# Kernel tuning notes

Hardware: AMD Instinct MI355X
Metric: run time of the kernel (lower is better)

The kernel has to match this reference:

```python
import jax, jax.numpy as jnp
import numpy as np

DIM = 2048
NUM_HEADS = 16
HEAD_DIM = DIM // NUM_HEADS  # 128


def setup_inputs() -> dict:
    key = jax.random.key(0)
    ks = jax.random.split(key, 5)
    scale = 0.02
    x = jax.random.normal(ks[0], (1, 2048, DIM), dtype=jnp.float32)
    # nn.Linear weights stored as [out_features, in_features]
    Wq = jax.random.normal(ks[1], (DIM, DIM), dtype=jnp.float32) * scale
    Wk = jax.random.normal(ks[2], (HEAD_DIM, DIM), dtype=jnp.float32) * scale
    Wv = jax.random.normal(ks[3], (HEAD_DIM, DIM), dtype=jnp.float32) * scale
    Wo = jax.random.normal(ks[4], (DIM, DIM), dtype=jnp.float32) * scale
    return {"x": x, "Wq": Wq, "Wk": Wk, "Wv": Wv, "Wo": Wo}


def reference(x, Wq, Wk, Wv, Wo):
    batch, seq_len, dim = x.shape
    q = x @ Wq.T                                   # [b, s, dim]
    k = x @ Wk.T                                   # [b, s, head_dim] (shared across heads)
    v = x @ Wv.T                                   # [b, s, head_dim]
    q = q.reshape(batch, seq_len, NUM_HEADS, HEAD_DIM).transpose(0, 2, 1, 3)  # [b, h, s, d]
    # MQA: single KV head broadcast across query heads (no materialized repeat)
    scores = jnp.einsum("bhqd,bkd->bhqk", q, k) / (HEAD_DIM ** 0.5)
    probs = jax.nn.softmax(scores, axis=-1)        # [b, h, q, k]
    out = jnp.einsum("bhqk,bkd->bhqd", probs, v)   # [b, h, s, d]
    out = out.transpose(0, 2, 1, 3).reshape(batch, seq_len, dim)
    return out @ Wo.T
```

## Files before the change

### kernel.cpp

```cpp
#include <hip/hip_runtime.h>

typedef float  float4_t __attribute__((ext_vector_type(4)));
typedef __bf16 bf16x8   __attribute__((ext_vector_type(8)));
typedef unsigned short u16;

__device__ __forceinline__ u16 f2bf(float f) {
    unsigned u = __float_as_uint(f);
    u += 0x7fffu + ((u >> 16) & 1u);
    return (u16)(u >> 16);
}

#define GLOAD_LDS16(g, l)                                              \
    __builtin_amdgcn_global_load_lds(                                  \
        (__attribute__((address_space(1))) void*)(g),                  \
        (__attribute__((address_space(3))) void*)(l), 16, 0, 0)

__global__ __launch_bounds__(256) void cast_kernel(const float* __restrict__ in,
                                                   u16* __restrict__ out, int n4) {
    int i = blockIdx.x * 256 + threadIdx.x;
    if (i >= n4) return;
    float4 f = ((const float4*)in)[i];
    ushort4 r;
    r.x = f2bf(f.x); r.y = f2bf(f.y); r.z = f2bf(f.z); r.w = f2bf(f.w);
    ((ushort4*)out)[i] = r;
}

template <typename EPI>
__device__ __forceinline__ void gemm_core(const u16* __restrict__ A,
                                          const u16* __restrict__ B,
                                          int K, int bm, int bn, EPI epi) {
    __shared__ __align__(16) u16 As[128 * 32];
    __shared__ __align__(16) u16 Bs[128 * 32];
    const int tid  = threadIdx.x;
    const int lane = tid & 63, wave = tid >> 6;
    const int wm = wave >> 1, wn = wave & 1;
    const int quad = lane >> 4, l16 = lane & 15;

    float4_t acc[4][4] = {};
    const int r0 = tid >> 2;
    const int c0 = (tid & 3) * 8;

    for (int k0 = 0; k0 < K; k0 += 32) {
#pragma unroll
        for (int i = 0; i < 2; ++i) {
            const int row = i * 64 + r0;
            const int e   = (i * 256 + tid) * 8;
            GLOAD_LDS16(A + (size_t)(bm + row) * K + k0 + c0, &As[e]);
            GLOAD_LDS16(B + (size_t)(bn + row) * K + k0 + c0, &Bs[e]);
        }
        __syncthreads();

        bf16x8 af[4], bfr[4];
#pragma unroll
        for (int mi = 0; mi < 4; ++mi)
            af[mi] = *(const bf16x8*)&As[(wm * 64 + mi * 16 + l16) * 32 + quad * 8];
#pragma unroll
        for (int ni = 0; ni < 4; ++ni)
            bfr[ni] = *(const bf16x8*)&Bs[(wn * 64 + ni * 16 + l16) * 32 + quad * 8];
#pragma unroll
        for (int mi = 0; mi < 4; ++mi)
#pragma unroll
            for (int ni = 0; ni < 4; ++ni)
                acc[mi][ni] = __builtin_amdgcn_mfma_f32_16x16x32_bf16(
                    af[mi], bfr[ni], acc[mi][ni], 0, 0, 0);
        __syncthreads();
    }

#pragma unroll
    for (int mi = 0; mi < 4; ++mi) {
        const int row = bm + wm * 64 + mi * 16 + quad * 4;
#pragma unroll
        for (int ni = 0; ni < 4; ++ni) {
            const int col = bn + wn * 64 + ni * 16 + l16;
#pragma unroll
            for (int r = 0; r < 4; ++r) epi(row + r, col, acc[mi][ni][r]);
        }
    }
}

__global__ __launch_bounds__(256) void gemm_qkv(const u16* __restrict__ A,
                                                const u16* __restrict__ B,
                                                u16* __restrict__ qb,
                                                u16* __restrict__ kb,
                                                u16* __restrict__ vtb) {
    gemm_core(A, B, 2048, blockIdx.x * 128, blockIdx.y * 128,
              [=](int row, int col, float v) {
                  if (col < 2048)
                      qb[(size_t)row * 2048 + col] = f2bf(v * 0.08838834764831845f);
                  else if (col < 2176)
                      kb[(size_t)row * 128 + (col - 2048)] = f2bf(v);
                  else
                      vtb[(size_t)(col - 2176) * 2048 + row] = f2bf(v);
              });
}

__global__ __launch_bounds__(256) void gemm_out(const u16* __restrict__ A,
                                                const u16* __restrict__ B,
                                                float* __restrict__ C) {
    gemm_core(A, B, 2048, blockIdx.x * 128, blockIdx.y * 128,
              [=](int row, int col, float v) {
                  C[(size_t)row * 2048 + col] = v;
              });
}

__global__ __launch_bounds__(256) void mqa_attn(const u16* __restrict__ Q,
                                                const u16* __restrict__ Kmat,
                                                const u16* __restrict__ Vt,
                                                u16* __restrict__ O) {
    __shared__ __align__(16) u16 Ks[2][4][64 * 32];
    __shared__ __align__(16) u16 Vts[2][2][128 * 32];
    __shared__ __align__(16) u16 Ps[4][32 * 72];
    const int tid  = threadIdx.x;
    const int wave = tid >> 6, lane = tid & 63;
    const int quad = lane >> 4, l16 = lane & 15;
    const int h     = blockIdx.y;
    const int qbase = blockIdx.x * 128 + wave * 32;

    const int kr = tid >> 2, kc = (tid & 3) * 8;

    bf16x8 qf[2][4];
#pragma unroll
    for (int mt = 0; mt < 2; ++mt)
#pragma unroll
        for (int kb4 = 0; kb4 < 4; ++kb4)
            qf[mt][kb4] = *(const bf16x8*)(Q + (size_t)(qbase + mt * 16 + l16) * 2048 +
                                           h * 128 + kb4 * 32 + quad * 8);

    float4_t acc[2][8];
#pragma unroll
    for (int mt = 0; mt < 2; ++mt)
#pragma unroll
        for (int nt = 0; nt < 8; ++nt) acc[mt][nt] = (float4_t){0.f, 0.f, 0.f, 0.f};
    float lsum[8] = {};

    u16* pb = Ps[wave];

#pragma unroll
    for (int kb4 = 0; kb4 < 4; ++kb4)
        GLOAD_LDS16(Kmat + (size_t)kr * 128 + kb4 * 32 + kc, &Ks[0][kb4][tid * 8]);
#pragma unroll
    for (int kk = 0; kk < 2; ++kk)
#pragma unroll
        for (int h2 = 0; h2 < 2; ++h2)
            GLOAD_LDS16(Vt + (size_t)(h2 * 64 + kr) * 2048 + kk * 32 + kc,
                        &Vts[0][kk][(h2 * 64 + kr) * 32 + kc]);
    __syncthreads();

    int buf = 0;
    for (int s = 0; s < 32; ++s) {
        const int k0 = s * 64;
        if (s < 31) {
            const int kn = k0 + 64;
#pragma unroll
            for (int kb4 = 0; kb4 < 4; ++kb4)
                GLOAD_LDS16(Kmat + (size_t)(kn + kr) * 128 + kb4 * 32 + kc,
                            &Ks[buf ^ 1][kb4][tid * 8]);
#pragma unroll
            for (int kk = 0; kk < 2; ++kk)
#pragma unroll
                for (int h2 = 0; h2 < 2; ++h2)
                    GLOAD_LDS16(Vt + (size_t)(h2 * 64 + kr) * 2048 + kn + kk * 32 + kc,
                                &Vts[buf ^ 1][kk][(h2 * 64 + kr) * 32 + kc]);
        }

#pragma unroll
        for (int ct = 0; ct < 4; ++ct) {
            float4_t s0 = (float4_t){0.f, 0.f, 0.f, 0.f};
            float4_t s1 = (float4_t){0.f, 0.f, 0.f, 0.f};
#pragma unroll
            for (int kb4 = 0; kb4 < 4; ++kb4) {
                bf16x8 kf = *(const bf16x8*)&Ks[buf][kb4][(ct * 16 + l16) * 32 + quad * 8];
                s0 = __builtin_amdgcn_mfma_f32_16x16x32_bf16(qf[0][kb4], kf, s0, 0, 0, 0);
                s1 = __builtin_amdgcn_mfma_f32_16x16x32_bf16(qf[1][kb4], kf, s1, 0, 0, 0);
            }
#pragma unroll
            for (int r = 0; r < 4; ++r) {
                const float e0 = __expf(s0[r]);
                const float e1 = __expf(s1[r]);
                lsum[r]     += e0;
                lsum[4 + r] += e1;
                pb[(quad * 4 + r) * 72 + ct * 16 + l16]        = f2bf(e0);
                pb[(16 + quad * 4 + r) * 72 + ct * 16 + l16]   = f2bf(e1);
            }
        }
        bf16x8 pa[2][2];
#pragma unroll
        for (int mt = 0; mt < 2; ++mt)
#pragma unroll
            for (int kk = 0; kk < 2; ++kk)
                pa[mt][kk] = *(const bf16x8*)&pb[(mt * 16 + l16) * 72 + kk * 32 + quad * 8];
#pragma unroll
        for (int kk = 0; kk < 2; ++kk)
#pragma unroll
            for (int nt = 0; nt < 8; ++nt) {
                bf16x8 vf = *(const bf16x8*)&Vts[buf][kk][(nt * 16 + l16) * 32 + quad * 8];
                acc[0][nt] = __builtin_amdgcn_mfma_f32_16x16x32_bf16(pa[0][kk], vf, acc[0][nt], 0, 0, 0);
                acc[1][nt] = __builtin_amdgcn_mfma_f32_16x16x32_bf16(pa[1][kk], vf, acc[1][nt], 0, 0, 0);
            }
        __syncthreads();
        buf ^= 1;
    }

#pragma unroll
    for (int mt = 0; mt < 2; ++mt)
#pragma unroll
        for (int r = 0; r < 4; ++r) {
            float lrow = lsum[mt * 4 + r];
#pragma unroll
            for (int off = 1; off < 16; off <<= 1) lrow += __shfl_xor(lrow, off);
            const float inv = 1.0f / lrow;
            const size_t rowoff = (size_t)(qbase + mt * 16 + quad * 4 + r) * 2048 + h * 128;
#pragma unroll
            for (int nt = 0; nt < 8; ++nt)
                O[rowoff + nt * 16 + l16] = f2bf(acc[mt][nt][r] * inv);
        }
}

extern "C" void kernel_launch(void* const* d_in, const int* in_sizes, int n_in,
                              void* d_out, int out_size, void* d_ws, size_t ws_size,
                              hipStream_t stream) {
    const float* x  = (const float*)d_in[0];
    const float* Wq = (const float*)d_in[1];
    const float* Wk = (const float*)d_in[2];
    const float* Wv = (const float*)d_in[3];
    const float* Wo = (const float*)d_in[4];
    float* out = (float*)d_out;

    u16* ws   = (u16*)d_ws;
    u16* xb   = ws;
    u16* Wqb  = xb  + (4 << 20);
    u16* Wkb  = Wqb + (4 << 20);
    u16* Wvb  = Wkb + (256 << 10);
    u16* Wob  = Wvb + (256 << 10);
    u16* qb   = Wob + (4 << 20);
    u16* kb   = qb  + (4 << 20);
    u16* vtb  = kb  + (256 << 10);
    u16* attn = vtb + (256 << 10);

    cast_kernel<<<4096, 256, 0, stream>>>(x,  xb,  1 << 20);
    cast_kernel<<<4096, 256, 0, stream>>>(Wq, Wqb, 1 << 20);
    cast_kernel<<<256,  256, 0, stream>>>(Wk, Wkb, 1 << 16);
    cast_kernel<<<256,  256, 0, stream>>>(Wv, Wvb, 1 << 16);
    cast_kernel<<<4096, 256, 0, stream>>>(Wo, Wob, 1 << 20);

    gemm_qkv<<<dim3(16, 18), 256, 0, stream>>>(xb, Wqb, qb, kb, vtb);
    mqa_attn<<<dim3(16, 16), 256, 0, stream>>>(qb, kb, vtb, attn);
    gemm_out<<<dim3(16, 16), 256, 0, stream>>>(attn, Wob, out);
}
```

Measured before the change: 264.5 us.

## Fuse cast launches and shrink attention blocks to 128 threads without double buffering

Merges the five fp32-to-bf16 cast launches into a single kernel that picks its source tensor from the block index, removing per-launch overhead. The attention kernel now runs 64 query rows per 128-thread block, doubling the grid to 512 blocks for better CU coverage on the 256-CU part. It drops K/V double buffering in favour of single-buffered loads followed by a barrier. This lowers LDS use per block but exposes global load latency unless other resident blocks hide it, and each K/V tile is now loaded twice as often across the grid.

```diff
diff --git a/kernel.cpp b/kernel.cpp
--- a/kernel.cpp
+++ b/kernel.cpp
@@ -15,14 +15,27 @@
         (__attribute__((address_space(1))) void*)(g),                  \
         (__attribute__((address_space(3))) void*)(l), 16, 0, 0)
 
-__global__ __launch_bounds__(256) void cast_kernel(const float* __restrict__ in,
-                                                   u16* __restrict__ out, int n4) {
-    int i = blockIdx.x * 256 + threadIdx.x;
-    if (i >= n4) return;
-    float4 f = ((const float4*)in)[i];
+__global__ __launch_bounds__(256) void cast_all(const float* __restrict__ x,
+                                                const float* __restrict__ wq,
+                                                const float* __restrict__ wk,
+                                                const float* __restrict__ wv,
+                                                const float* __restrict__ wo,
+                                                u16* __restrict__ xb, u16* __restrict__ wqb,
+                                                u16* __restrict__ wkb, u16* __restrict__ wvb,
+                                                u16* __restrict__ wob) {
+    const int b = blockIdx.x;
+    const float* src;
+    u16* dst;
+    int i;
+    if (b < 4096)      { src = x;  dst = xb;  i = b * 256 + threadIdx.x; }
+    else if (b < 8192) { src = wq; dst = wqb; i = (b - 4096) * 256 + threadIdx.x; }
+    else if (b < 8448) { src = wk; dst = wkb; i = (b - 8192) * 256 + threadIdx.x; }
+    else if (b < 8704) { src = wv; dst = wvb; i = (b - 8448) * 256 + threadIdx.x; }
+    else               { src = wo; dst = wob; i = (b - 8704) * 256 + threadIdx.x; }
+    float4 f = ((const float4*)src)[i];
     ushort4 r;
     r.x = f2bf(f.x); r.y = f2bf(f.y); r.z = f2bf(f.z); r.w = f2bf(f.w);
-    ((ushort4*)out)[i] = r;
+    ((ushort4*)dst)[i] = r;
 }
 
 template <typename EPI>
@@ -103,20 +116,18 @@
               });
 }
 
-__global__ __launch_bounds__(256) void mqa_attn(const u16* __restrict__ Q,
-                                                const u16* __restrict__ Kmat,
-                                                const u16* __restrict__ Vt,
-                                                u16* __restrict__ O) {
-    __shared__ __align__(16) u16 Ks[2][4][64 * 32];
-    __shared__ __align__(16) u16 Vts[2][2][128 * 32];
-    __shared__ __align__(16) u16 Ps[4][32 * 72];
+__global__ __launch_bounds__(128, 2) void mqa_attn(const u16* __restrict__ Q,
+                                                   const u16* __restrict__ Kmat,
+                                                   const u16* __restrict__ Vt,
+                                                   u16* __restrict__ O) {
+    __shared__ __align__(16) u16 Ks[4 * 64 * 32];
+    __shared__ __align__(16) u16 Vts[2 * 128 * 32];
+    __shared__ __align__(16) u16 Ps[2][32 * 72];
     const int tid  = threadIdx.x;
     const int wave = tid >> 6, lane = tid & 63;
     const int quad = lane >> 4, l16 = lane & 15;
     const int h     = blockIdx.y;
-    const int qbase = blockIdx.x * 128 + wave * 32;
-
-    const int kr = tid >> 2, kc = (tid & 3) * 8;
+    const int qbase = blockIdx.x * 64 + wave * 32;
 
     bf16x8 qf[2][4];
 #pragma unroll
@@ -135,33 +146,23 @@
 
     u16* pb = Ps[wave];
 
-#pragma unroll
-    for (int kb4 = 0; kb4 < 4; ++kb4)
-        GLOAD_LDS16(Kmat + (size_t)kr * 128 + kb4 * 32 + kc, &Ks[0][kb4][tid * 8]);
-#pragma unroll
-    for (int kk = 0; kk < 2; ++kk)
-#pragma unroll
-        for (int h2 = 0; h2 < 2; ++h2)
-            GLOAD_LDS16(Vt + (size_t)(h2 * 64 + kr) * 2048 + kk * 32 + kc,
-                        &Vts[0][kk][(h2 * 64 + kr) * 32 + kc]);
-    __syncthreads();
-
-    int buf = 0;
     for (int s = 0; s < 32; ++s) {
         const int k0 = s * 64;
-        if (s < 31) {
-            const int kn = k0 + 64;
-#pragma unroll
-            for (int kb4 = 0; kb4 < 4; ++kb4)
-                GLOAD_LDS16(Kmat + (size_t)(kn + kr) * 128 + kb4 * 32 + kc,
-                            &Ks[buf ^ 1][kb4][tid * 8]);
-#pragma unroll
-            for (int kk = 0; kk < 2; ++kk)
-#pragma unroll
-                for (int h2 = 0; h2 < 2; ++h2)
-                    GLOAD_LDS16(Vt + (size_t)(h2 * 64 + kr) * 2048 + kn + kk * 32 + kc,
-                                &Vts[buf ^ 1][kk][(h2 * 64 + kr) * 32 + kc]);
-        }
+#pragma unroll
+        for (int i = 0; i < 8; ++i) {
+            const int slot = i * 128 + tid;
+            const int sub = slot >> 8, win = slot & 255;
+            const int row = win >> 2, ch = (win & 3) * 8;
+            GLOAD_LDS16(Kmat + (size_t)(k0 + row) * 128 + sub * 32 + ch, &Ks[slot * 8]);
+        }
+#pragma unroll
+        for (int i = 0; i < 8; ++i) {
+            const int slot = i * 128 + tid;
+            const int sub = slot >> 9, win = slot & 511;
+            const int row = win >> 2, ch = (win & 3) * 8;
+            GLOAD_LDS16(Vt + (size_t)row * 2048 + k0 + sub * 32 + ch, &Vts[slot * 8]);
+        }
+        __syncthreads();
 
 #pragma unroll
         for (int ct = 0; ct < 4; ++ct) {
@@ -169,7 +170,7 @@
             float4_t s1 = (float4_t){0.f, 0.f, 0.f, 0.f};
 #pragma unroll
             for (int kb4 = 0; kb4 < 4; ++kb4) {
-                bf16x8 kf = *(const bf16x8*)&Ks[buf][kb4][(ct * 16 + l16) * 32 + quad * 8];
+                bf16x8 kf = *(const bf16x8*)&Ks[(kb4 * 64 + ct * 16 + l16) * 32 + quad * 8];
                 s0 = __builtin_amdgcn_mfma_f32_16x16x32_bf16(qf[0][kb4], kf, s0, 0, 0, 0);
                 s1 = __builtin_amdgcn_mfma_f32_16x16x32_bf16(qf[1][kb4], kf, s1, 0, 0, 0);
             }
@@ -179,8 +180,8 @@
                 const float e1 = __expf(s1[r]);
                 lsum[r]     += e0;
                 lsum[4 + r] += e1;
-                pb[(quad * 4 + r) * 72 + ct * 16 + l16]        = f2bf(e0);
-                pb[(16 + quad * 4 + r) * 72 + ct * 16 + l16]   = f2bf(e1);
+                pb[(quad * 4 + r) * 72 + ct * 16 + l16]      = f2bf(e0);
+                pb[(16 + quad * 4 + r) * 72 + ct * 16 + l16] = f2bf(e1);
             }
         }
         bf16x8 pa[2][2];
@@ -193,12 +194,11 @@
         for (int kk = 0; kk < 2; ++kk)
 #pragma unroll
             for (int nt = 0; nt < 8; ++nt) {
-                bf16x8 vf = *(const bf16x8*)&Vts[buf][kk][(nt * 16 + l16) * 32 + quad * 8];
+                bf16x8 vf = *(const bf16x8*)&Vts[(kk * 128 + nt * 16 + l16) * 32 + quad * 8];
                 acc[0][nt] = __builtin_amdgcn_mfma_f32_16x16x32_bf16(pa[0][kk], vf, acc[0][nt], 0, 0, 0);
                 acc[1][nt] = __builtin_amdgcn_mfma_f32_16x16x32_bf16(pa[1][kk], vf, acc[1][nt], 0, 0, 0);
             }
         __syncthreads();
-        buf ^= 1;
     }
 
 #pragma unroll
@@ -237,13 +237,9 @@
     u16* vtb  = kb  + (256 << 10);
     u16* attn = vtb + (256 << 10);
 
-    cast_kernel<<<4096, 256, 0, stream>>>(x,  xb,  1 << 20);
-    cast_kernel<<<4096, 256, 0, stream>>>(Wq, Wqb, 1 << 20);
-    cast_kernel<<<256,  256, 0, stream>>>(Wk, Wkb, 1 << 16);
-    cast_kernel<<<256,  256, 0, stream>>>(Wv, Wvb, 1 << 16);
-    cast_kernel<<<4096, 256, 0, stream>>>(Wo, Wob, 1 << 20);
+    cast_all<<<12800, 256, 0, stream>>>(x, Wq, Wk, Wv, Wo, xb, Wqb, Wkb, Wvb, Wob);
 
     gemm_qkv<<<dim3(16, 18), 256, 0, stream>>>(xb, Wqb, qb, kb, vtb);
-    mqa_attn<<<dim3(16, 16), 256, 0, stream>>>(qb, kb, vtb, attn);
+    mqa_attn<<<dim3(32, 16), 128, 0, stream>>>(qb, kb, vtb, attn);
     gemm_out<<<dim3(16, 16), 256, 0, stream>>>(attn, Wob, out);
 }
```

Measured after the change: 260.5 us. Within noise of the previous version (-1.5%).
